# Optimization experiments

Measured on AMD Instinct MI355X. Metric: run time of the kernel, lower is better.

The kernel has to match this reference:

```python
import jax, jax.numpy as jnp
import numpy as np

H, DH, M = 8, 64, 3          # heads, dim_head, num memory tokens
DIM = 512                    # model dim
INNER = H * DH               # 512
SCALE = DH ** -0.5
SQRT_DH = float(np.sqrt(DH))
SQRT_M = float(np.sqrt(M))


def setup_inputs() -> dict:
    key = jax.random.key(0)
    ks = jax.random.split(key, 7)
    b, n = 2, 2048
    x = jax.random.normal(ks[0], (b, n, DIM), dtype=jnp.float32)
    # Linear weights stored as (in, out); y = x @ W
    wq = jax.random.normal(ks[1], (DIM, INNER), dtype=jnp.float32) * (DIM ** -0.5)
    wkv = jax.random.normal(ks[2], (DIM, 2 * INNER), dtype=jnp.float32) * (DIM ** -0.5)
    wo = jax.random.normal(ks[3], (INNER, DIM), dtype=jnp.float32) * (INNER ** -0.5)
    bo = jnp.zeros((DIM,), dtype=jnp.float32)
    # xavier_normal_ std = sqrt(2 / (fan_in + fan_out)) over last two dims (M, INNER)
    xav = float(np.sqrt(2.0 / (M + INNER)))
    m_k = jax.random.normal(ks[4], (1, M, INNER), dtype=jnp.float32) * xav
    m_v = jax.random.normal(ks[5], (1, M, INNER), dtype=jnp.float32) * xav
    return {"x": x, "wq": wq, "wkv": wkv, "wo": wo, "bo": bo, "m_k": m_k, "m_v": m_v}


def reference(x, wq, wkv, wo, bo, m_k, m_v):
    b, n, _ = x.shape
    # projections -> (b, h, n, d)
    q = (x @ wq).reshape(b, n, H, DH).transpose(0, 2, 1, 3)
    kv = x @ wkv
    k, v = jnp.split(kv, 2, axis=-1)
    k = k.reshape(b, n, H, DH).transpose(0, 2, 1, 3)
    v = v.reshape(b, n, H, DH).transpose(0, 2, 1, 3)
    # memory tokens: torch does expand(b, M, INNER).view(b, H, M, DH),
    # a flat reshape (NOT a per-head rearrange) -- replicate exactly.
    mk = SQRT_DH * jnp.broadcast_to(m_k, (b, M, INNER)).reshape(b, H, M, DH)
    mv = SQRT_M * jnp.broadcast_to(m_v, (b, M, INNER)).reshape(b, H, M, DH)
    k = jnp.concatenate([k, mk], axis=2)  # (b, h, n+M, d)
    v = jnp.concatenate([v, mv], axis=2)
    dots = jnp.einsum('bhid,bhjd->bhij', q, k) * SCALE  # (b, h, n, n+M)
    attn = jax.nn.softmax(dots, axis=-1)                # dropout = identity (eval)
    out = jnp.einsum('bhij,bhjd->bhid', attn, v)
    out = out.transpose(0, 2, 1, 3).reshape(b, n, INNER)
    return out @ wo + bo
```

## Files before the change

kernel.cpp:

```cpp
#include <hip/hip_runtime.h>

typedef unsigned short u16;
typedef unsigned int u32;
typedef __attribute__((ext_vector_type(8))) __bf16 bf16x8;
typedef __attribute__((ext_vector_type(4))) float f32x4;

#define DEVI __device__ __forceinline__
#define C1 0.180336880f
#define C2 (-23.0831200f)

DEVI float bf2f(u16 u) {
    unsigned int v = ((unsigned int)u) << 16;
    return __uint_as_float(v);
}
DEVI u16 f2bf(float f) {
    unsigned int x = __float_as_uint(f);
    x += 0x7fffu + ((x >> 16) & 1u);
    return (u16)(x >> 16);
}
DEVI u32 pk2(float lo, float hi) {
    union { __bf16 b[2]; u32 u; } c;
    c.b[0] = (__bf16)lo; c.b[1] = (__bf16)hi;
    return c.u;
}
DEVI bf16x8 ldb8(const u16* p) {
    union { uint4 u; bf16x8 b; } c;
    c.u = *(const uint4*)p;
    return c.b;
}
DEVI f32x4 mfma32(bf16x8 a, bf16x8 b, f32x4 c) {
    return __builtin_amdgcn_mfma_f32_16x16x32_bf16(a, b, c, 0, 0, 0);
}
DEVI float clamp4(float v) { return fminf(fmaxf(v, -1e4f), 1e4f); }
DEVI float fexp2(float x) { return __builtin_amdgcn_exp2f(x); }
DEVI void gld16(const u16* g, u16* l) {
    __builtin_amdgcn_global_load_lds(
        (const __attribute__((address_space(1))) void*)g,
        (__attribute__((address_space(3))) void*)l, 16, 0, 0);
}

__global__ __launch_bounds__(256) void prep(
    const float* __restrict__ wq, const float* __restrict__ wkv,
    const float* __restrict__ wo, const float* __restrict__ x,
    const float* __restrict__ mkf, const float* __restrict__ mvf,
    u16* __restrict__ wqkvT, u16* __restrict__ woT, u16* __restrict__ xb,
    u16* __restrict__ qkv)
{
    const int bid = blockIdx.x, tid = threadIdx.x;
    if (bid < 256) {
        __shared__ u16 T[64][68];
        int j0, k0; const float* W; int ldw; u16* Out;
        if (bid < 192) { int jt = bid % 24, kt = bid / 24;
            j0 = jt * 64; k0 = kt * 64;
            if (j0 < 512) { W = wq + j0;          ldw = 512;  }
            else          { W = wkv + (j0 - 512); ldw = 1024; }
            Out = wqkvT;
        } else { int t = bid - 192;
            j0 = (t >> 3) * 64; k0 = (t & 7) * 64;
            W = wo + j0; ldw = 512; Out = woT;
        }
        const int lr = tid >> 4, lc = tid & 15;
        #pragma unroll
        for (int i = 0; i < 4; ++i) {
            int k = lr + i * 16;
            float4 v = *(const float4*)(W + (size_t)(k0 + k) * ldw + lc * 4);
            u16 p[4] = { f2bf(v.x), f2bf(v.y), f2bf(v.z), f2bf(v.w) };
            *(uint2*)&T[k][lc * 4] = *(uint2*)p;
        }
        __syncthreads();
        #pragma unroll
        for (int i = 0; i < 4; ++i) {
            int j = lr + i * 16;
            u16 p[4];
            #pragma unroll
            for (int c = 0; c < 4; ++c) p[c] = T[lc * 4 + c][j];
            *(uint2*)(Out + (size_t)(j0 + j) * 512 + k0 + lc * 4) = *(uint2*)p;
        }
    } else if (bid < 2304) {
        int e = (bid - 256) * 1024 + tid * 4;
        float4 v = *(const float4*)(x + e);
        u16 p[4] = { f2bf(v.x), f2bf(v.y), f2bf(v.z), f2bf(v.w) };
        *(uint2*)(xb + e) = *(uint2*)p;
    } else {
        int e = (bid - 2304) * 256 + tid;
        int b = e >> 16, rem = e & 65535;
        int row2 = rem >> 10, c = rem & 1023;
        float v = 0.f;
        if (row2 < 3) {
            int hh = (c & 511) >> 6, d = c & 63;
            int src = hh * 192 + row2 * 64 + d;
            v = (c < 512) ? 8.0f * mkf[src] : 1.7320508f * mvf[src];
        }
        qkv[((size_t)b * 2112 + 2048 + row2) * 1536 + 512 + c] = f2bf(v);
    }
}

template<int TM, int TN, bool F32OUT, bool FM>
__global__ __launch_bounds__(256) void gemmK(
    const u16* __restrict__ A, int lda,
    const u16* __restrict__ BT, int ldb,
    void* __restrict__ Cv, int ldc,
    const float* __restrict__ bias, int K, int mpad,
    const u16* __restrict__ Op, const float* __restrict__ Lp)
{
    constexpr int IL = TM / 32, JL = TN / 32;
    __shared__ u16 As0[TM * 32], As1[TM * 32];
    __shared__ u16 Bs0[TN * 32], Bs1[TN * 32];

    const int tid = threadIdx.x;
    const int m0 = blockIdx.x * TM, n0 = blockIdx.y * TN;
    const int w = tid >> 6, lane = tid & 63, l15 = lane & 15, quad = lane >> 4;
    const int wr = w >> 1, wc = w & 1;
    const int sr = lane >> 2, sc = (lane & 3) * 8;

    f32x4 acc[IL][JL];
    #pragma unroll
    for (int i = 0; i < IL; ++i)
        #pragma unroll
        for (int j = 0; j < JL; ++j) acc[i][j] = (f32x4){0.f, 0.f, 0.f, 0.f};

    for (int k0 = 0; k0 < K; k0 += 64) {
        __syncthreads();
        if constexpr (!FM) {
            #pragma unroll
            for (int p = 0; p < TM / 64; ++p) {
                int r0 = w * (TM / 4) + p * 16;
                const u16* g = A + (size_t)(m0 + r0 + sr) * lda + k0 + sc;
                gld16(g,      &As0[r0 * 32]);
                gld16(g + 32, &As1[r0 * 32]);
            }
        } else {
            const int h = k0 >> 6;
            #pragma unroll
            for (int p = 0; p < TM / 64; ++p) {
                int r0 = w * (TM / 4) + p * 16;
                int row = m0 + r0 + sr;
                float l = Lp[(size_t)row * 8 + h]
                        + Lp[((size_t)4096  + row) * 8 + h]
                        + Lp[((size_t)8192  + row) * 8 + h]
                        + Lp[((size_t)12288 + row) * 8 + h];
                float rl = 1.0f / fmaxf(l, 1e-30f);
                const u16* g = Op + (size_t)row * 512 + k0 + sc;
                #pragma unroll
                for (int hf = 0; hf < 2; ++hf) {
                    const u16* gh = g + hf * 32;
                    float a8[8] = {0.f,0.f,0.f,0.f,0.f,0.f,0.f,0.f};
                    #pragma unroll
                    for (int sl = 0; sl < 4; ++sl) {
                        uint4 pv = *(const uint4*)(gh + (size_t)sl * 2097152);
                        a8[0] += bf2f((u16)(pv.x & 0xffff)); a8[1] += bf2f((u16)(pv.x >> 16));
                        a8[2] += bf2f((u16)(pv.y & 0xffff)); a8[3] += bf2f((u16)(pv.y >> 16));
                        a8[4] += bf2f((u16)(pv.z & 0xffff)); a8[5] += bf2f((u16)(pv.z >> 16));
                        a8[6] += bf2f((u16)(pv.w & 0xffff)); a8[7] += bf2f((u16)(pv.w >> 16));
                    }
                    u16 ob[8];
                    #pragma unroll
                    for (int i = 0; i < 8; ++i) ob[i] = f2bf(clamp4(a8[i] * rl));
                    u16* dst = (hf ? As1 : As0) + (r0 + sr) * 32 + sc;
                    *(uint4*)dst = *(uint4*)ob;
                }
            }
        }
        #pragma unroll
        for (int p = 0; p < TN / 64; ++p) {
            int r0 = w * (TN / 4) + p * 16;
            const u16* g = BT + (size_t)(n0 + r0 + sr) * ldb + k0 + sc;
            gld16(g,      &Bs0[r0 * 32]);
            gld16(g + 32, &Bs1[r0 * 32]);
        }
        __syncthreads();

        #pragma unroll
        for (int ks = 0; ks < 2; ++ks) {
            const u16* Asel = ks ? As1 : As0;
            const u16* Bsel = ks ? Bs1 : Bs0;
            bf16x8 af[IL], bf[JL];
            #pragma unroll
            for (int i = 0; i < IL; ++i)
                af[i] = ldb8(&Asel[(wr * (TM / 2) + 16 * i + l15) * 32 + quad * 8]);
            #pragma unroll
            for (int j = 0; j < JL; ++j)
                bf[j] = ldb8(&Bsel[(wc * (TN / 2) + 16 * j + l15) * 32 + quad * 8]);
            #pragma unroll
            for (int i = 0; i < IL; ++i)
                #pragma unroll
                for (int j = 0; j < JL; ++j)
                    acc[i][j] = mfma32(af[i], bf[j], acc[i][j]);
        }
    }

    #pragma unroll
    for (int j = 0; j < JL; ++j) {
        int col = n0 + wc * (TN / 2) + 16 * j + l15;
        float bv = bias ? bias[col] : 0.f;
        #pragma unroll
        for (int i = 0; i < IL; ++i) {
            #pragma unroll
            for (int r = 0; r < 4; ++r) {
                int row = m0 + wr * (TM / 2) + 16 * i + quad * 4 + r;
                int orow = row + ((row >> 11) * mpad);
                float vr = clamp4(acc[i][j][r] + bv);
                if (F32OUT) ((float*)Cv)[(size_t)orow * ldc + col] = vr;
                else        ((u16*)Cv)[(size_t)orow * ldc + col] = f2bf(vr);
            }
        }
    }
}

__global__ __launch_bounds__(256, 4) void attn_kernel(
    const u16* __restrict__ qkv, u16* __restrict__ Opart,
    float* __restrict__ Lpart)
{
    __shared__ alignas(16) u16 Ks[64][72];
    __shared__ alignas(16) u16 Vt[64][72];
    __shared__ alignas(16) u16 Ps[128][72];

    const int tid = threadIdx.x;
    const int bx = blockIdx.x;
    const int qt = bx >> 2, s = bx & 3;
    const int h = blockIdx.y, b = blockIdx.z;
    const int w = tid >> 6, lane = tid & 63, l15 = lane & 15, quad = lane >> 4;
    const size_t bq = (size_t)b * 2112;
    const int rq = qt * 128;
    const int ro = b * 2048 + qt * 128;

    union { u32 u[4]; bf16x8 b8; } onesu;
    #pragma unroll
    for (int i = 0; i < 4; ++i) onesu.u[i] = 0x3F803F80u;
    const bf16x8 onesf = onesu.b8;

    {
        int row = tid >> 1, cg = (tid & 1) * 32;
        const u16* src = qkv + (bq + rq + row) * 1536 + h * 64 + cg;
        *(uint4*)&Ps[row][cg]      = *(const uint4*)src;
        *(uint4*)&Ps[row][cg + 8]  = *(const uint4*)(src + 8);
        *(uint4*)&Ps[row][cg + 16] = *(const uint4*)(src + 16);
        *(uint4*)&Ps[row][cg + 24] = *(const uint4*)(src + 24);
    }
    __syncthreads();
    bf16x8 qf[2][2];
    #pragma unroll
    for (int sub = 0; sub < 2; ++sub) {
        qf[sub][0] = ldb8(&Ps[64 * sub + 16 * w + l15][quad * 8]);
        qf[sub][1] = ldb8(&Ps[64 * sub + 16 * w + l15][32 + quad * 8]);
    }

    f32x4 Od[2][4], Ol[2];
    #pragma unroll
    for (int sub = 0; sub < 2; ++sub) {
        #pragma unroll
        for (int t = 0; t < 4; ++t) Od[sub][t] = (f32x4){0.f, 0.f, 0.f, 0.f};
        Ol[sub] = (f32x4){0.f, 0.f, 0.f, 0.f};
    }

    const int krow = tid >> 2, kcg = (tid & 3) * 16;
    const int vkp = (tid & 31) * 2, vdg = ((tid >> 5) & 7) * 8;

    const int kt0 = s ? 8 * s + 1 : 0;
    const int kt1 = 8 * s + 9;
    for (int kt = kt0; kt < kt1; ++kt) {
        const u16* ksrc = qkv + (bq + kt * 64 + krow) * 1536 + 512 + h * 64 + kcg;
        uint4 k0 = *(const uint4*)ksrc, k1 = *(const uint4*)(ksrc + 8);
        const u16* vsrc = qkv + (bq + kt * 64 + vkp) * 1536 + 1024 + h * 64 + vdg;
        uint4 v0 = *(const uint4*)vsrc, v1 = *(const uint4*)(vsrc + 1536);
        __syncthreads();
        *(uint4*)&Ks[krow][kcg]     = k0;
        *(uint4*)&Ks[krow][kcg + 8] = k1;
        {
            u32 a0[4] = {v0.x, v0.y, v0.z, v0.w};
            u32 a1[4] = {v1.x, v1.y, v1.z, v1.w};
            #pragma unroll
            for (int i = 0; i < 4; ++i) {
                u32 lo = __builtin_amdgcn_perm(a1[i], a0[i], 0x05040100u);
                u32 hi = __builtin_amdgcn_perm(a1[i], a0[i], 0x07060302u);
                *(u32*)&Vt[vdg + 2 * i][vkp]     = lo;
                *(u32*)&Vt[vdg + 2 * i + 1][vkp] = hi;
            }
        }
        __syncthreads();

        f32x4 d[2][4];
        #pragma unroll
        for (int sub = 0; sub < 2; ++sub)
            #pragma unroll
            for (int t = 0; t < 4; ++t) d[sub][t] = (f32x4){0.f, 0.f, 0.f, 0.f};
        #pragma unroll
        for (int ks = 0; ks < 2; ++ks) {
            #pragma unroll
            for (int t = 0; t < 4; ++t) {
                bf16x8 kf = ldb8(&Ks[16 * t + l15][ks * 32 + quad * 8]);
                d[0][t] = mfma32(kf, qf[0][ks], d[0][t]);
                d[1][t] = mfma32(kf, qf[1][ks], d[1][t]);
            }
        }
        if (kt == 32) {
            #pragma unroll
            for (int sub = 0; sub < 2; ++sub) {
                #pragma unroll
                for (int t = 1; t < 4; ++t)
                    d[sub][t] = (f32x4){-1e9f, -1e9f, -1e9f, -1e9f};
                #pragma unroll
                for (int r = 0; r < 4; ++r)
                    if (!(quad == 0 && r < 3)) d[sub][0][r] = -1e9f;
            }
        }

        #pragma unroll
        for (int sub = 0; sub < 2; ++sub)
            #pragma unroll
            for (int t = 0; t < 4; ++t) {
                uint2 pv = { pk2(fexp2(fmaf(d[sub][t][0], C1, C2)),
                                 fexp2(fmaf(d[sub][t][1], C1, C2))),
                             pk2(fexp2(fmaf(d[sub][t][2], C1, C2)),
                                 fexp2(fmaf(d[sub][t][3], C1, C2))) };
                *(uint2*)&Ps[64 * sub + 16 * w + l15][16 * t + 4 * quad] = pv;
            }
        #pragma unroll
        for (int ks = 0; ks < 2; ++ks) {
            bf16x8 af0 = ldb8(&Ps[16 * w + l15][ks * 32 + quad * 8]);
            bf16x8 af1 = ldb8(&Ps[64 + 16 * w + l15][ks * 32 + quad * 8]);
            #pragma unroll
            for (int dt = 0; dt < 4; ++dt) {
                bf16x8 vf = ldb8(&Vt[16 * dt + l15][ks * 32 + quad * 8]);
                Od[0][dt] = mfma32(af0, vf, Od[0][dt]);
                Od[1][dt] = mfma32(af1, vf, Od[1][dt]);
            }
            Ol[0] = mfma32(af0, onesf, Ol[0]);
            Ol[1] = mfma32(af1, onesf, Ol[1]);
        }
    }

    u16* Ob = Opart + (size_t)s * 4096 * 512;
    #pragma unroll
    for (int sub = 0; sub < 2; ++sub) {
        #pragma unroll
        for (int r = 0; r < 4; ++r) {
            int row = ro + 64 * sub + 16 * w + quad * 4 + r;
            #pragma unroll
            for (int dt = 0; dt < 4; ++dt) {
                int col = h * 64 + 16 * dt + l15;
                Ob[(size_t)row * 512 + col] = f2bf(Od[sub][dt][r]);
            }
            if (l15 == 0)
                Lpart[((size_t)s * 4096 + row) * 8 + h] = Ol[sub][r];
        }
    }
}

extern "C" void kernel_launch(void* const* d_in, const int* in_sizes, int n_in,
                              void* d_out, int out_size, void* d_ws, size_t ws_size,
                              hipStream_t stream)
{
    (void)in_sizes; (void)n_in; (void)out_size; (void)ws_size;
    const float* x   = (const float*)d_in[0];
    const float* wq  = (const float*)d_in[1];
    const float* wkv = (const float*)d_in[2];
    const float* wo  = (const float*)d_in[3];
    const float* bo  = (const float*)d_in[4];
    const float* mk  = (const float*)d_in[5];
    const float* mv  = (const float*)d_in[6];
    float* out = (float*)d_out;

    u16* qkv    = (u16*)d_ws;
    u16* woT    = qkv + 6488064;
    u16* wqkvT  = woT + 262144;
    u16* xb     = wqkvT + 786432;
    u16* Opart  = xb + 2097152;
    float* Lpart = (float*)(Opart + 8388608);

    prep<<<2816, 256, 0, stream>>>(wq, wkv, wo, x, mk, mv, wqkvT, woT, xb, qkv);
    gemmK<128, 64, false, false><<<dim3(32, 24), 256, 0, stream>>>(
        xb, 512, wqkvT, 512, qkv, 1536, nullptr, 512, 64, nullptr, nullptr);
    attn_kernel<<<dim3(64, 8, 2), 256, 0, stream>>>(qkv, Opart, Lpart);
    gemmK<64, 64, true, true><<<dim3(64, 8), 256, 0, stream>>>(
        nullptr, 512, woT, 512, out, 512, bo, 512, 0, Opart, Lpart);
}
```

Measured before the change: 131.5 us.

## Split attention KV into five slabs and XOR-swizzle LDS tiles

The attention kernel now splits the key range into five slabs instead of four (7/7/7/6/6 key tiles), giving more blocks and a higher occupancy hint of 5 per CU. The combine step in the output GEMM sums five partial O and L slabs. The padded shared-memory arrays are replaced with unpadded 64-wide rows using an XOR swizzle, which cuts LDS footprint and is meant to avoid bank conflicts. In exchange, the output GEMM reads one more partial slab per row, and more partial-output workspace is needed.

```diff
diff --git a/kernel.cpp b/kernel.cpp
--- a/kernel.cpp
+++ b/kernel.cpp
@@ -8,6 +8,8 @@
 #define DEVI __device__ __forceinline__
 #define C1 0.180336880f
 #define C2 (-23.0831200f)
+
+#define NSLAB 5
 
 DEVI float bf2f(u16 u) {
     unsigned int v = ((unsigned int)u) << 16;
@@ -37,6 +39,9 @@
     __builtin_amdgcn_global_load_lds(
         (const __attribute__((address_space(1))) void*)g,
         (__attribute__((address_space(3))) void*)l, 16, 0, 0);
+}
+DEVI int swz(int r, int c) {
+    return (r << 6) + ((((c >> 3) ^ r) & 7) << 3) + (c & 7);
 }
 
 __global__ __launch_bounds__(256) void prep(
@@ -135,10 +140,10 @@
             for (int p = 0; p < TM / 64; ++p) {
                 int r0 = w * (TM / 4) + p * 16;
                 int row = m0 + r0 + sr;
-                float l = Lp[(size_t)row * 8 + h]
-                        + Lp[((size_t)4096  + row) * 8 + h]
-                        + Lp[((size_t)8192  + row) * 8 + h]
-                        + Lp[((size_t)12288 + row) * 8 + h];
+                float l = 0.f;
+                #pragma unroll
+                for (int sl = 0; sl < NSLAB; ++sl)
+                    l += Lp[((size_t)sl * 4096 + row) * 8 + h];
                 float rl = 1.0f / fmaxf(l, 1e-30f);
                 const u16* g = Op + (size_t)row * 512 + k0 + sc;
                 #pragma unroll
@@ -146,7 +151,7 @@
                     const u16* gh = g + hf * 32;
                     float a8[8] = {0.f,0.f,0.f,0.f,0.f,0.f,0.f,0.f};
                     #pragma unroll
-                    for (int sl = 0; sl < 4; ++sl) {
+                    for (int sl = 0; sl < NSLAB; ++sl) {
                         uint4 pv = *(const uint4*)(gh + (size_t)sl * 2097152);
                         a8[0] += bf2f((u16)(pv.x & 0xffff)); a8[1] += bf2f((u16)(pv.x >> 16));
                         a8[2] += bf2f((u16)(pv.y & 0xffff)); a8[3] += bf2f((u16)(pv.y >> 16));
@@ -207,17 +212,17 @@
     }
 }
 
-__global__ __launch_bounds__(256, 4) void attn_kernel(
+__global__ __launch_bounds__(256, 5) void attn_kernel(
     const u16* __restrict__ qkv, u16* __restrict__ Opart,
     float* __restrict__ Lpart)
 {
-    __shared__ alignas(16) u16 Ks[64][72];
-    __shared__ alignas(16) u16 Vt[64][72];
-    __shared__ alignas(16) u16 Ps[128][72];
+    __shared__ alignas(16) u16 Ks[4096];
+    __shared__ alignas(16) u16 Vt[4096];
+    __shared__ alignas(16) u16 Ps[8192];
 
     const int tid = threadIdx.x;
     const int bx = blockIdx.x;
-    const int qt = bx >> 2, s = bx & 3;
+    const int qt = bx / 5, s = bx - qt * 5;
     const int h = blockIdx.y, b = blockIdx.z;
     const int w = tid >> 6, lane = tid & 63, l15 = lane & 15, quad = lane >> 4;
     const size_t bq = (size_t)b * 2112;
@@ -232,17 +237,17 @@
     {
         int row = tid >> 1, cg = (tid & 1) * 32;
         const u16* src = qkv + (bq + rq + row) * 1536 + h * 64 + cg;
-        *(uint4*)&Ps[row][cg]      = *(const uint4*)src;
-        *(uint4*)&Ps[row][cg + 8]  = *(const uint4*)(src + 8);
-        *(uint4*)&Ps[row][cg + 16] = *(const uint4*)(src + 16);
-        *(uint4*)&Ps[row][cg + 24] = *(const uint4*)(src + 24);
+        *(uint4*)&Ps[swz(row, cg)]      = *(const uint4*)src;
+        *(uint4*)&Ps[swz(row, cg + 8)]  = *(const uint4*)(src + 8);
+        *(uint4*)&Ps[swz(row, cg + 16)] = *(const uint4*)(src + 16);
+        *(uint4*)&Ps[swz(row, cg + 24)] = *(const uint4*)(src + 24);
     }
     __syncthreads();
     bf16x8 qf[2][2];
     #pragma unroll
     for (int sub = 0; sub < 2; ++sub) {
-        qf[sub][0] = ldb8(&Ps[64 * sub + 16 * w + l15][quad * 8]);
-        qf[sub][1] = ldb8(&Ps[64 * sub + 16 * w + l15][32 + quad * 8]);
+        qf[sub][0] = ldb8(&Ps[swz(64 * sub + 16 * w + l15, quad * 8)]);
+        qf[sub][1] = ldb8(&Ps[swz(64 * sub + 16 * w + l15, 32 + quad * 8)]);
     }
 
     f32x4 Od[2][4], Ol[2];
@@ -256,16 +261,16 @@
     const int krow = tid >> 2, kcg = (tid & 3) * 16;
     const int vkp = (tid & 31) * 2, vdg = ((tid >> 5) & 7) * 8;
 
-    const int kt0 = s ? 8 * s + 1 : 0;
-    const int kt1 = 8 * s + 9;
+    const int kt0 = (s < 4) ? 7 * s : 27;
+    const int kt1 = (s < 3) ? 7 * s + 7 : ((s == 3) ? 27 : 33);
     for (int kt = kt0; kt < kt1; ++kt) {
         const u16* ksrc = qkv + (bq + kt * 64 + krow) * 1536 + 512 + h * 64 + kcg;
         uint4 k0 = *(const uint4*)ksrc, k1 = *(const uint4*)(ksrc + 8);
         const u16* vsrc = qkv + (bq + kt * 64 + vkp) * 1536 + 1024 + h * 64 + vdg;
         uint4 v0 = *(const uint4*)vsrc, v1 = *(const uint4*)(vsrc + 1536);
         __syncthreads();
-        *(uint4*)&Ks[krow][kcg]     = k0;
-        *(uint4*)&Ks[krow][kcg + 8] = k1;
+        *(uint4*)&Ks[swz(krow, kcg)]     = k0;
+        *(uint4*)&Ks[swz(krow, kcg + 8)] = k1;
         {
             u32 a0[4] = {v0.x, v0.y, v0.z, v0.w};
             u32 a1[4] = {v1.x, v1.y, v1.z, v1.w};
@@ -273,8 +278,8 @@
             for (int i = 0; i < 4; ++i) {
                 u32 lo = __builtin_amdgcn_perm(a1[i], a0[i], 0x05040100u);
                 u32 hi = __builtin_amdgcn_perm(a1[i], a0[i], 0x07060302u);
-                *(u32*)&Vt[vdg + 2 * i][vkp]     = lo;
-                *(u32*)&Vt[vdg + 2 * i + 1][vkp] = hi;
+                *(u32*)&Vt[swz(vdg + 2 * i,     vkp)] = lo;
+                *(u32*)&Vt[swz(vdg + 2 * i + 1, vkp)] = hi;
             }
         }
         __syncthreads();
@@ -288,7 +293,7 @@
         for (int ks = 0; ks < 2; ++ks) {
             #pragma unroll
             for (int t = 0; t < 4; ++t) {
-                bf16x8 kf = ldb8(&Ks[16 * t + l15][ks * 32 + quad * 8]);
+                bf16x8 kf = ldb8(&Ks[swz(16 * t + l15, ks * 32 + quad * 8)]);
                 d[0][t] = mfma32(kf, qf[0][ks], d[0][t]);
                 d[1][t] = mfma32(kf, qf[1][ks], d[1][t]);
             }
@@ -313,15 +318,15 @@
                                  fexp2(fmaf(d[sub][t][1], C1, C2))),
                              pk2(fexp2(fmaf(d[sub][t][2], C1, C2)),
                                  fexp2(fmaf(d[sub][t][3], C1, C2))) };
-                *(uint2*)&Ps[64 * sub + 16 * w + l15][16 * t + 4 * quad] = pv;
+                *(uint2*)&Ps[swz(64 * sub + 16 * w + l15, 16 * t + 4 * quad)] = pv;
             }
         #pragma unroll
         for (int ks = 0; ks < 2; ++ks) {
-            bf16x8 af0 = ldb8(&Ps[16 * w + l15][ks * 32 + quad * 8]);
-            bf16x8 af1 = ldb8(&Ps[64 + 16 * w + l15][ks * 32 + quad * 8]);
+            bf16x8 af0 = ldb8(&Ps[swz(16 * w + l15,      ks * 32 + quad * 8)]);
+            bf16x8 af1 = ldb8(&Ps[swz(64 + 16 * w + l15, ks * 32 + quad * 8)]);
             #pragma unroll
             for (int dt = 0; dt < 4; ++dt) {
-                bf16x8 vf = ldb8(&Vt[16 * dt + l15][ks * 32 + quad * 8]);
+                bf16x8 vf = ldb8(&Vt[swz(16 * dt + l15, ks * 32 + quad * 8)]);
                 Od[0][dt] = mfma32(af0, vf, Od[0][dt]);
                 Od[1][dt] = mfma32(af1, vf, Od[1][dt]);
             }
@@ -366,12 +371,12 @@
     u16* wqkvT  = woT + 262144;
     u16* xb     = wqkvT + 786432;
     u16* Opart  = xb + 2097152;
-    float* Lpart = (float*)(Opart + 8388608);
+    float* Lpart = (float*)(Opart + (size_t)NSLAB * 2097152);
 
     prep<<<2816, 256, 0, stream>>>(wq, wkv, wo, x, mk, mv, wqkvT, woT, xb, qkv);
     gemmK<128, 64, false, false><<<dim3(32, 24), 256, 0, stream>>>(
         xb, 512, wqkvT, 512, qkv, 1536, nullptr, 512, 64, nullptr, nullptr);
-    attn_kernel<<<dim3(64, 8, 2), 256, 0, stream>>>(qkv, Opart, Lpart);
+    attn_kernel<<<dim3(16 * NSLAB, 8, 2), 256, 0, stream>>>(qkv, Opart, Lpart);
     gemmK<64, 64, true, true><<<dim3(64, 8), 256, 0, stream>>>(
         nullptr, 512, woT, 512, out, 512, bo, 512, 0, Opart, Lpart);
 }
```

Result: slower. 234.4 us (+78.3%).
